# Performance work log

Hardware: AMD Instinct MI355X
Metric: run time of the kernel (lower is better)

The kernel has to match this reference:

```python
import jax, jax.numpy as jnp
import numpy as np

B, S, D = 8, 2048, 512

def setup_inputs() -> dict:
    key = jax.random.key(0)
    ks = jax.random.split(key, 4)
    scale = 1.0 / np.sqrt(D)
    x = jax.random.normal(ks[0], (B, S, D), dtype=jnp.float32)
    Wq = jax.random.normal(ks[1], (D, D), dtype=jnp.float32) * scale
    Wk = jax.random.normal(ks[2], (D, D), dtype=jnp.float32) * scale
    Wv = jax.random.normal(ks[3], (D, D), dtype=jnp.float32) * scale
    bq = jnp.zeros((D,), jnp.float32)
    bk = jnp.zeros((D,), jnp.float32)
    bv = jnp.zeros((D,), jnp.float32)
    return {"x": x, "Wq": Wq, "bq": bq, "Wk": Wk, "bk": bk, "Wv": Wv, "bv": bv}

def reference(x, Wq, bq, Wk, bk, Wv, bv):
    # Q, K, V projections: [B,S,D]
    Q = jnp.einsum('bsd,de->bse', x, Wq) + bq
    K = jnp.einsum('bsd,de->bse', x, Wk) + bk
    V = jnp.einsum('bsd,de->bse', x, Wv) + bv
    scale = jnp.sqrt(jnp.asarray(Q.shape[-1], Q.dtype))
    scores = jnp.einsum('bqd,bkd->bqk', Q, K) / scale  # [B,S,S]
    attn = jax.nn.softmax(scores, axis=-1)
    context = jnp.einsum('bqk,bkd->bqd', attn, V)  # [B,S,D]
    return context
```

## Files before the change

### kernel.cpp

```cpp
#include <hip/hip_runtime.h>
#include <hip/hip_bf16.h>

#define B_ 8
#define S_ 2048
#define D_ 512

typedef __attribute__((ext_vector_type(8))) short short8;
typedef __attribute__((ext_vector_type(4))) float f32x4;

static __device__ __forceinline__ unsigned short f2bf(float f) {
    union { float f; unsigned u; } v; v.f = f;
    unsigned r = v.u + 0x7FFFu + ((v.u >> 16) & 1u);
    return (unsigned short)(r >> 16);
}

static __device__ __forceinline__ float fexp2(float x) {
    float r; asm("v_exp_f32 %0, %1" : "=v"(r) : "v"(x)); return r;
}

static __device__ __forceinline__ void gl_lds16(const void* g, void* l) {
    __builtin_amdgcn_global_load_lds(
        (const __attribute__((address_space(1))) unsigned int*)g,
        (__attribute__((address_space(3))) unsigned int*)l, 16, 0, 0);
}

__global__ void k_prep(const float* __restrict__ x,
                       const float* __restrict__ Wq, const float* __restrict__ Wk,
                       const float* __restrict__ Wv,
                       unsigned short* __restrict__ xb, unsigned short* __restrict__ Wt,
                       float* __restrict__ l) {
    int bid = blockIdx.x;
    if (bid < 4096) {
        int i = bid * 256 + threadIdx.x;
        const float4* p = (const float4*)x + (size_t)i * 2;
        float4 a = p[0], b = p[1];
        union { unsigned short u[8]; uint4 v; } o;
        o.u[0] = f2bf(a.x); o.u[1] = f2bf(a.y); o.u[2] = f2bf(a.z); o.u[3] = f2bf(a.w);
        o.u[4] = f2bf(b.x); o.u[5] = f2bf(b.y); o.u[6] = f2bf(b.z); o.u[7] = f2bf(b.w);
        ((uint4*)xb)[i] = o.v;
    } else if (bid < 7168) {
        int idx = (bid - 4096) * 256 + threadIdx.x;
        int z = idx >> 18;
        int r = idx & 262143;
        int e = r >> 9, d = r & 511;
        const float* W = (z == 0) ? Wq : ((z == 1) ? Wk : Wv);
        Wt[idx] = f2bf(W[d * 512 + e]);
    } else {
        l[(bid - 7168) * 256 + threadIdx.x] = 0.f;
    }
}

__global__ __launch_bounds__(256, 4) void k_qkv(
    const unsigned short* __restrict__ xb, const unsigned short* __restrict__ Wt,
    const float* __restrict__ biasq, const float* __restrict__ biask,
    const float* __restrict__ biasv,
    unsigned short* __restrict__ Qb, unsigned short* __restrict__ Kb,
    unsigned short* __restrict__ Vs) {
  __shared__ __align__(16) unsigned char smA[16384];
  __shared__ __align__(16) unsigned char smB[16384];
  const int z = blockIdx.z;
  const unsigned short* W = Wt + (size_t)z * (D_ * D_);
  const int lane = threadIdx.x & 63, wid = threadIdx.x >> 6;
  const int c = lane & 15, g = lane >> 4;
  const int wr = wid >> 1, wc = wid & 1;
  const int m_blk = blockIdx.x * 128;
  const int n_blk = blockIdx.y * 128;

  const int src_sw = ((lane & 7) * 16) ^ (((lane >> 3) & 7) << 4);
  const unsigned char* ga = (const unsigned char*)xb
      + (size_t)(m_blk + wid * 32 + (lane >> 3)) * 1024;
  const unsigned char* gb = (const unsigned char*)W
      + (size_t)(n_blk + wid * 32 + (lane >> 3)) * 1024;
  unsigned char* la = smA + wid * 4096;
  unsigned char* lb = smB + wid * 4096;

  f32x4 acc[4][4];
#pragma unroll
  for (int mi = 0; mi < 4; ++mi)
#pragma unroll
    for (int ni = 0; ni < 4; ++ni) acc[mi][ni] = (f32x4){0.f, 0.f, 0.f, 0.f};

  for (int step = 0; step < 8; ++step) {
    __syncthreads();
#pragma unroll
    for (int i = 0; i < 4; ++i) {
      gl_lds16(ga + (size_t)i * 8192 + step * 128 + src_sw, la + i * 1024);
      gl_lds16(gb + (size_t)i * 8192 + step * 128 + src_sw, lb + i * 1024);
    }
    __syncthreads();
#pragma unroll
    for (int kc = 0; kc < 2; ++kc) {
      const int ro = (kc * 64 + g * 16) ^ ((c & 7) << 4);
      short8 af[4], bf[4];
#pragma unroll
      for (int mi = 0; mi < 4; ++mi)
        af[mi] = *(const short8*)(smA + (wr * 64 + mi * 16 + c) * 128 + ro);
#pragma unroll
      for (int ni = 0; ni < 4; ++ni)
        bf[ni] = *(const short8*)(smB + (wc * 64 + ni * 16 + c) * 128 + ro);
#pragma unroll
      for (int mi = 0; mi < 4; ++mi)
#pragma unroll
        for (int ni = 0; ni < 4; ++ni)
          acc[mi][ni] = __builtin_amdgcn_mfma_f32_16x16x32_bf16(af[mi], bf[ni], acc[mi][ni], 0, 0, 0);
    }
  }

  const int m0 = m_blk + wr * 64;
  const int n0 = n_blk + wc * 64;
  if (z < 2) {
    const float* bias = (z == 0) ? biasq : biask;
    unsigned short* outp = (z == 0) ? Qb : Kb;
    const float scl = (z == 0) ? 0.0637587238f : 1.0f;
#pragma unroll
    for (int ni = 0; ni < 4; ++ni) {
      int cc = n0 + ni * 16 + c;
      float bb = bias[cc];
#pragma unroll
      for (int mi = 0; mi < 4; ++mi)
#pragma unroll
        for (int r = 0; r < 4; ++r) {
          int row = m0 + mi * 16 + g * 4 + r;
          outp[(size_t)row * D_ + cc] = f2bf((acc[mi][ni][r] + bb) * scl);
        }
    }
  } else {
#pragma unroll
    for (int ni = 0; ni < 4; ++ni) {
      int e = n0 + ni * 16 + c;
      float bb = biasv[e];
#pragma unroll
      for (int mi = 0; mi < 4; ++mi) {
        int row = m0 + mi * 16 + g * 4;
        int bi = row >> 11, sl = row & 2047;
        int t = sl >> 5, kvin = sl & 31;
        union { unsigned short u[4]; uint2 v; } pk;
#pragma unroll
        for (int r = 0; r < 4; ++r) pk.u[r] = f2bf(acc[mi][ni][r] + bb);
        *(uint2*)(Vs + ((((size_t)bi * 64 + t) * 512) + e) * 32 + kvin) = pk.v;
      }
    }
  }
}

__global__ __launch_bounds__(256, 4) void k_pa(
    const unsigned short* __restrict__ Qb, const unsigned short* __restrict__ Kb,
    unsigned short* __restrict__ P, float* __restrict__ l,
    int b_base, int bc) {
  __shared__ __align__(16) unsigned char smA[16384];
  __shared__ __align__(16) unsigned char smB[16384];
  const int lane = threadIdx.x & 63, wid = threadIdx.x >> 6;
  const int c = lane & 15, g = lane >> 4;
  const int wr = wid >> 1, wc = wid & 1;
  const int bloc = blockIdx.x % bc;
  const int tile = blockIdx.x / bc;
  const int b = b_base + bloc;
  const int m_blk = (tile & 15) * 128;
  const int n_blk = (tile >> 4) * 128;
  unsigned short* Pb = P + (size_t)bloc * S_ * S_;

  const int src_sw = ((lane & 7) * 16) ^ (((lane >> 3) & 7) << 4);
  const unsigned char* ga = (const unsigned char*)(Kb + (size_t)b * S_ * D_)
      + (size_t)(m_blk + wid * 32 + (lane >> 3)) * 1024;
  const unsigned char* gb = (const unsigned char*)(Qb + (size_t)b * S_ * D_)
      + (size_t)(n_blk + wid * 32 + (lane >> 3)) * 1024;
  unsigned char* la = smA + wid * 4096;
  unsigned char* lb = smB + wid * 4096;

  f32x4 acc[4][4];
#pragma unroll
  for (int mi = 0; mi < 4; ++mi)
#pragma unroll
    for (int ni = 0; ni < 4; ++ni) acc[mi][ni] = (f32x4){0.f, 0.f, 0.f, 0.f};

  for (int step = 0; step < 8; ++step) {
    __syncthreads();
#pragma unroll
    for (int i = 0; i < 4; ++i) {
      gl_lds16(ga + (size_t)i * 8192 + step * 128 + src_sw, la + i * 1024);
      gl_lds16(gb + (size_t)i * 8192 + step * 128 + src_sw, lb + i * 1024);
    }
    __syncthreads();
#pragma unroll
    for (int kc = 0; kc < 2; ++kc) {
      const int ro = (kc * 64 + g * 16) ^ ((c & 7) << 4);
      short8 af[4], bf[4];
#pragma unroll
      for (int mi = 0; mi < 4; ++mi)
        af[mi] = *(const short8*)(smA + (wr * 64 + mi * 16 + c) * 128 + ro);
#pragma unroll
      for (int ni = 0; ni < 4; ++ni)
        bf[ni] = *(const short8*)(smB + (wc * 64 + ni * 16 + c) * 128 + ro);
#pragma unroll
      for (int mi = 0; mi < 4; ++mi)
#pragma unroll
        for (int ni = 0; ni < 4; ++ni)
          acc[mi][ni] = __builtin_amdgcn_mfma_f32_16x16x32_bf16(af[mi], bf[ni], acc[mi][ni], 0, 0, 0);
    }
  }

  const float SH = 11.5415603f;
  float psum[4] = {0.f, 0.f, 0.f, 0.f};
  __syncthreads();
#pragma unroll
  for (int ni = 0; ni < 4; ++ni) {
    const int q_loc = wc * 64 + ni * 16 + c;
#pragma unroll
    for (int mi = 0; mi < 4; ++mi) {
      float p0 = fexp2(acc[mi][ni][0] - SH);
      float p1 = fexp2(acc[mi][ni][1] - SH);
      float p2 = fexp2(acc[mi][ni][2] - SH);
      float p3 = fexp2(acc[mi][ni][3] - SH);
      psum[ni] += (p0 + p1) + (p2 + p3);
      unsigned w0, w1;
      asm("v_cvt_pk_bf16_f32 %0, %1, %2" : "=v"(w0) : "v"(p0), "v"(p1));
      asm("v_cvt_pk_bf16_f32 %0, %1, %2" : "=v"(w1) : "v"(p2), "v"(p3));
      const int kv2 = (wr * 64 + mi * 16 + g * 4) * 2;
      *(uint2*)(smA + q_loc * 256 + (kv2 ^ ((q_loc & 15) << 4))) = (uint2){w0, w1};
    }
  }
#pragma unroll
  for (int ni = 0; ni < 4; ++ni) {
    float v = psum[ni];
    v += __shfl_xor(v, 16);
    v += __shfl_xor(v, 32);
    if (g == 0)
      atomicAdd(l + b * S_ + n_blk + wc * 64 + ni * 16 + c, v);
  }
  __syncthreads();
#pragma unroll
  for (int i = 0; i < 8; ++i) {
    const int q_loc = wid * 32 + i * 4 + (lane >> 4);
    const int kvb = (lane & 15) * 16;
    uint4 v = *(const uint4*)(smA + q_loc * 256 + (kvb ^ ((q_loc & 15) << 4)));
    *(uint4*)((unsigned char*)Pb + (size_t)(n_blk + q_loc) * 4096 + m_blk * 2 + kvb) = v;
  }
}

__global__ __launch_bounds__(512, 1) void k_pb(
    const unsigned short* __restrict__ P, const unsigned short* __restrict__ Vs,
    const float* __restrict__ l, float* __restrict__ out,
    int b_base, int bc) {
  __shared__ __align__(16) unsigned char sm[147456];
  const int lane = threadIdx.x & 63, wid = threadIdx.x >> 6;
  const int c = lane & 15, g = lane >> 4;
  const int wm = wid >> 2, wn = wid & 3;
  const int bloc = blockIdx.x % bc;
  const int tile = blockIdx.x / bc;
  const int b = b_base + bloc;
  const int m_blk = (tile & 1) * 256;
  const int n_blk = (tile >> 1) * 128;
  const unsigned char* Pb = (const unsigned char*)(P + (size_t)bloc * S_ * S_);
  const unsigned char* Vsb = (const unsigned char*)(Vs + (size_t)b * 64 * 512 * 32);

  const int src_sw = ((lane & 7) * 16) ^ (((lane >> 3) & 7) << 4);
  const unsigned char* gA0 = Vsb + (size_t)(src_sw >> 6) * 32768
      + (size_t)(m_blk + (lane >> 3)) * 64 + (src_sw & 63);
  const unsigned char* gB0 = Pb + (size_t)(n_blk + (lane >> 3)) * 4096 + src_sw;

#define STG_A(h_, t_, bp_)                                                   \
  {                                                                          \
    _Pragma("unroll")                                                        \
    for (int i = 0; i < 2; ++i) {                                            \
      int rl = wid * 16 + i * 8;                                             \
      int pbv = (rl & 63) + ((rl & 64) << 1) + (h_) * 64;                    \
      gl_lds16(gA0 + (size_t)(t_) * 65536 + (size_t)pbv * 64,                \
               sm + (bp_) * 49152 + pbv * 128);                              \
    }                                                                        \
  }
#define STG_B(h_, t_, bp_)                                                   \
  {                                                                          \
    int rl = wid * 8;                                                        \
    int pbv = (rl & 8) + (h_) * 16 + ((rl >> 4) << 5);                       \
    gl_lds16(gB0 + (size_t)pbv * 4096 + (t_) * 128,                          \
             sm + (bp_) * 49152 + 32768 + pbv * 128);                        \
  }

  f32x4 acc[8][2];
#pragma unroll
  for (int a = 0; a < 8; ++a)
#pragma unroll
    for (int ni = 0; ni < 2; ++ni) acc[a][ni] = (f32x4){0.f, 0.f, 0.f, 0.f};

  STG_A(0, 0, 0); STG_B(0, 0, 0); STG_A(1, 0, 0); STG_B(1, 0, 0);
  STG_A(0, 1, 1); STG_B(0, 1, 1); STG_A(1, 1, 1); STG_B(1, 1, 1);

  for (int t = 0; t < 32; ++t) {
    const int cb = t % 3;
    const int nb = (t + 2) % 3;
    if (t < 31) asm volatile("s_waitcnt vmcnt(6)" ::: "memory");
    else        asm volatile("s_waitcnt vmcnt(0)" ::: "memory");
    __builtin_amdgcn_s_barrier();
    const unsigned char* Ab = sm + cb * 49152;
    const unsigned char* Bb = Ab + 32768;
    short8 bfr[2][2];
#pragma unroll
    for (int ni = 0; ni < 2; ++ni) {
      int row = wn * 32 + ni * 16 + c;
#pragma unroll
      for (int kc = 0; kc < 2; ++kc)
        bfr[ni][kc] = *(const short8*)(Bb + row * 128 + ((kc * 64 + g * 16) ^ ((c & 7) << 4)));
    }
    {
      short8 af[4][2];
#pragma unroll
      for (int mi = 0; mi < 4; ++mi) {
        int row = wm * 128 + mi * 16 + c;
#pragma unroll
        for (int kc = 0; kc < 2; ++kc)
          af[mi][kc] = *(const short8*)(Ab + row * 128 + ((kc * 64 + g * 16) ^ ((c & 7) << 4)));
      }
      if (t < 30) { STG_A(0, t + 2, nb); STG_B(0, t + 2, nb); }
      __builtin_amdgcn_s_setprio(1);
#pragma unroll
      for (int kc = 0; kc < 2; ++kc)
#pragma unroll
        for (int mi = 0; mi < 4; ++mi)
#pragma unroll
          for (int ni = 0; ni < 2; ++ni)
            acc[mi][ni] = __builtin_amdgcn_mfma_f32_16x16x32_bf16(af[mi][kc], bfr[ni][kc], acc[mi][ni], 0, 0, 0);
      __builtin_amdgcn_s_setprio(0);
    }
    {
      short8 af[4][2];
#pragma unroll
      for (int mi = 0; mi < 4; ++mi) {
        int row = wm * 128 + 64 + mi * 16 + c;
#pragma unroll
        for (int kc = 0; kc < 2; ++kc)
          af[mi][kc] = *(const short8*)(Ab + row * 128 + ((kc * 64 + g * 16) ^ ((c & 7) << 4)));
      }
      if (t < 30) { STG_A(1, t + 2, nb); STG_B(1, t + 2, nb); }
      __builtin_amdgcn_s_setprio(1);
#pragma unroll
      for (int kc = 0; kc < 2; ++kc)
#pragma unroll
        for (int mi = 0; mi < 4; ++mi)
#pragma unroll
          for (int ni = 0; ni < 2; ++ni)
            acc[4 + mi][ni] = __builtin_amdgcn_mfma_f32_16x16x32_bf16(af[mi][kc], bfr[ni][kc], acc[4 + mi][ni], 0, 0, 0);
      __builtin_amdgcn_s_setprio(0);
    }
  }
#undef STG_A
#undef STG_B

  float* ob = out + (size_t)b * S_ * D_;
#pragma unroll
  for (int ni = 0; ni < 2; ++ni) {
    const int q = n_blk + wn * 32 + ni * 16 + c;
    const float inv = 1.f / l[b * S_ + q];
#pragma unroll
    for (int a = 0; a < 8; ++a) {
      const int d0 = m_blk + wm * 128 + (a >> 2) * 64 + (a & 3) * 16 + g * 4;
      float4 v;
      v.x = acc[a][ni][0] * inv; v.y = acc[a][ni][1] * inv;
      v.z = acc[a][ni][2] * inv; v.w = acc[a][ni][3] * inv;
      *(float4*)(ob + (size_t)q * D_ + d0) = v;
    }
  }
}

extern "C" void kernel_launch(void* const* d_in, const int* in_sizes, int n_in,
                              void* d_out, int out_size, void* d_ws, size_t ws_size,
                              hipStream_t stream) {
  const float* x  = (const float*)d_in[0];
  const float* Wq = (const float*)d_in[1];
  const float* bq = (const float*)d_in[2];
  const float* Wk = (const float*)d_in[3];
  const float* bk = (const float*)d_in[4];
  const float* Wv = (const float*)d_in[5];
  const float* bv = (const float*)d_in[6];
  float* out = (float*)d_out;

  unsigned short* xb = (unsigned short*)d_ws;
  unsigned short* Wt = xb + (size_t)16384 * 512;
  unsigned short* Qb = Wt + (size_t)3 * 512 * 512;
  unsigned short* Kb = Qb + (size_t)16384 * 512;
  unsigned short* Vs = Kb + (size_t)16384 * 512;
  float* l = (float*)(Vs + (size_t)8 * 64 * 512 * 32);
  unsigned short* Pfull = (unsigned short*)(l + 8 * 2048);
  const size_t full_need =
      (size_t)((unsigned char*)(Pfull + (size_t)8 * 2048 * 2048) - (unsigned char*)d_ws);

  k_prep<<<dim3(7232), dim3(256), 0, stream>>>(x, Wq, Wk, Wv, xb, Wt, l);
  k_qkv<<<dim3(128, 4, 3), dim3(256), 0, stream>>>(xb, Wt, bq, bk, bv, Qb, Kb, Vs);

  if (ws_size >= full_need) {
    k_pa<<<dim3(2048), dim3(256), 0, stream>>>(Qb, Kb, Pfull, l, 0, 8);
    k_pb<<<dim3(256),  dim3(512), 0, stream>>>(Pfull, Vs, l, out, 0, 8);
  } else {
    unsigned short* P2 = xb;
    for (int g2 = 0; g2 < 4; ++g2) {
      k_pa<<<dim3(512), dim3(256), 0, stream>>>(Qb, Kb, P2, l, g2 * 2, 2);
      k_pb<<<dim3(64), dim3(512), 0, stream>>>(P2, Vs, l, out, g2 * 2, 2);
    }
  }
}
```

Baseline: 119.5 us.

## Restructure score kernel to 256x128 tiles with triple-buffered async LDS pipeline

The QK^T/exp kernel moves from 128x128 tiles on 256-thread blocks with two barriers per K-step to 256x128 tiles on 512-thread blocks. K and Q chunks are loaded into a three-stage LDS ring with global-to-LDS copies issued two steps ahead, and partial vmcnt waits keep loads in flight. It also raises MFMA priority around the math bursts. The goal is to hide global load latency and improve reuse per block, at the cost of one block per CU with about 144KB of LDS and lower occupancy.

```diff
diff --git a/kernel.cpp b/kernel.cpp
--- a/kernel.cpp
+++ b/kernel.cpp
@@ -143,96 +143,146 @@
   }
 }
 
-__global__ __launch_bounds__(256, 4) void k_pa(
+__global__ __launch_bounds__(512, 1) void k_pa(
     const unsigned short* __restrict__ Qb, const unsigned short* __restrict__ Kb,
     unsigned short* __restrict__ P, float* __restrict__ l,
     int b_base, int bc) {
-  __shared__ __align__(16) unsigned char smA[16384];
-  __shared__ __align__(16) unsigned char smB[16384];
+  __shared__ __align__(16) unsigned char sm[147456];
   const int lane = threadIdx.x & 63, wid = threadIdx.x >> 6;
   const int c = lane & 15, g = lane >> 4;
-  const int wr = wid >> 1, wc = wid & 1;
+  const int wm = wid >> 2, wn = wid & 3;
   const int bloc = blockIdx.x % bc;
   const int tile = blockIdx.x / bc;
   const int b = b_base + bloc;
-  const int m_blk = (tile & 15) * 128;
-  const int n_blk = (tile >> 4) * 128;
+  const int m_blk = (tile & 7) * 256;
+  const int n_blk = (tile >> 3) * 128;
   unsigned short* Pb = P + (size_t)bloc * S_ * S_;
 
   const int src_sw = ((lane & 7) * 16) ^ (((lane >> 3) & 7) << 4);
-  const unsigned char* ga = (const unsigned char*)(Kb + (size_t)b * S_ * D_)
-      + (size_t)(m_blk + wid * 32 + (lane >> 3)) * 1024;
-  const unsigned char* gb = (const unsigned char*)(Qb + (size_t)b * S_ * D_)
-      + (size_t)(n_blk + wid * 32 + (lane >> 3)) * 1024;
-  unsigned char* la = smA + wid * 4096;
-  unsigned char* lb = smB + wid * 4096;
-
-  f32x4 acc[4][4];
-#pragma unroll
-  for (int mi = 0; mi < 4; ++mi)
-#pragma unroll
-    for (int ni = 0; ni < 4; ++ni) acc[mi][ni] = (f32x4){0.f, 0.f, 0.f, 0.f};
-
-  for (int step = 0; step < 8; ++step) {
-    __syncthreads();
-#pragma unroll
-    for (int i = 0; i < 4; ++i) {
-      gl_lds16(ga + (size_t)i * 8192 + step * 128 + src_sw, la + i * 1024);
-      gl_lds16(gb + (size_t)i * 8192 + step * 128 + src_sw, lb + i * 1024);
-    }
-    __syncthreads();
-#pragma unroll
-    for (int kc = 0; kc < 2; ++kc) {
-      const int ro = (kc * 64 + g * 16) ^ ((c & 7) << 4);
-      short8 af[4], bf[4];
-#pragma unroll
-      for (int mi = 0; mi < 4; ++mi)
-        af[mi] = *(const short8*)(smA + (wr * 64 + mi * 16 + c) * 128 + ro);
-#pragma unroll
-      for (int ni = 0; ni < 4; ++ni)
-        bf[ni] = *(const short8*)(smB + (wc * 64 + ni * 16 + c) * 128 + ro);
-#pragma unroll
-      for (int mi = 0; mi < 4; ++mi)
-#pragma unroll
-        for (int ni = 0; ni < 4; ++ni)
-          acc[mi][ni] = __builtin_amdgcn_mfma_f32_16x16x32_bf16(af[mi], bf[ni], acc[mi][ni], 0, 0, 0);
-    }
-  }
-
+  const unsigned char* gA0 = (const unsigned char*)(Kb + (size_t)b * S_ * D_)
+      + (size_t)(m_blk + (lane >> 3)) * 1024 + src_sw;
+  const unsigned char* gB0 = (const unsigned char*)(Qb + (size_t)b * S_ * D_)
+      + (size_t)(n_blk + (lane >> 3)) * 1024 + src_sw;
+
+#define STG_A(h_, t_, bp_)                                                   \
+  {                                                                          \
+    _Pragma("unroll")                                                        \
+    for (int i = 0; i < 2; ++i) {                                            \
+      int r0 = (h_) * 128 + wid * 16 + i * 8;                                \
+      gl_lds16(gA0 + (size_t)r0 * 1024 + (t_) * 128,                         \
+               sm + (bp_) * 49152 + r0 * 128);                               \
+    }                                                                        \
+  }
+#define STG_B(h_, t_, bp_)                                                   \
+  {                                                                          \
+    int r0 = (h_) * 64 + wid * 8;                                            \
+    gl_lds16(gB0 + (size_t)r0 * 1024 + (t_) * 128,                           \
+             sm + (bp_) * 49152 + 32768 + r0 * 128);                         \
+  }
+
+  f32x4 acc[8][2];
+#pragma unroll
+  for (int a = 0; a < 8; ++a)
+#pragma unroll
+    for (int ni = 0; ni < 2; ++ni) acc[a][ni] = (f32x4){0.f, 0.f, 0.f, 0.f};
+
+  STG_A(0, 0, 0); STG_B(0, 0, 0); STG_A(1, 0, 0); STG_B(1, 0, 0);
+  STG_A(0, 1, 1); STG_B(0, 1, 1); STG_A(1, 1, 1); STG_B(1, 1, 1);
+
+  for (int t = 0; t < 8; ++t) {
+    const int cb = t % 3;
+    const int nb = (t + 2) % 3;
+    if (t < 7) asm volatile("s_waitcnt vmcnt(6)" ::: "memory");
+    else       asm volatile("s_waitcnt vmcnt(0)" ::: "memory");
+    __builtin_amdgcn_s_barrier();
+    const unsigned char* Ab = sm + cb * 49152;
+    const unsigned char* Bb = Ab + 32768;
+    short8 bfr[2][2];
+#pragma unroll
+    for (int ni = 0; ni < 2; ++ni) {
+      int row = wn * 32 + ni * 16 + c;
+#pragma unroll
+      for (int kc = 0; kc < 2; ++kc)
+        bfr[ni][kc] = *(const short8*)(Bb + row * 128 + ((kc * 64 + g * 16) ^ ((c & 7) << 4)));
+    }
+    {
+      short8 af[4][2];
+#pragma unroll
+      for (int mi = 0; mi < 4; ++mi) {
+        int row = wm * 128 + mi * 16 + c;
+#pragma unroll
+        for (int kc = 0; kc < 2; ++kc)
+          af[mi][kc] = *(const short8*)(Ab + row * 128 + ((kc * 64 + g * 16) ^ ((c & 7) << 4)));
+      }
+      if (t < 6) { STG_A(0, t + 2, nb); STG_B(0, t + 2, nb); }
+      __builtin_amdgcn_s_setprio(1);
+#pragma unroll
+      for (int kc = 0; kc < 2; ++kc)
+#pragma unroll
+        for (int mi = 0; mi < 4; ++mi)
+#pragma unroll
+          for (int ni = 0; ni < 2; ++ni)
+            acc[mi][ni] = __builtin_amdgcn_mfma_f32_16x16x32_bf16(af[mi][kc], bfr[ni][kc], acc[mi][ni], 0, 0, 0);
+      __builtin_amdgcn_s_setprio(0);
+    }
+    {
+      short8 af[4][2];
+#pragma unroll
+      for (int mi = 0; mi < 4; ++mi) {
+        int row = wm * 128 + 64 + mi * 16 + c;
+#pragma unroll
+        for (int kc = 0; kc < 2; ++kc)
+          af[mi][kc] = *(const short8*)(Ab + row * 128 + ((kc * 64 + g * 16) ^ ((c & 7) << 4)));
+      }
+      if (t < 6) { STG_A(1, t + 2, nb); STG_B(1, t + 2, nb); }
+      __builtin_amdgcn_s_setprio(1);
+#pragma unroll
+      for (int kc = 0; kc < 2; ++kc)
+#pragma unroll
+        for (int mi = 0; mi < 4; ++mi)
+#pragma unroll
+          for (int ni = 0; ni < 2; ++ni)
+            acc[4 + mi][ni] = __builtin_amdgcn_mfma_f32_16x16x32_bf16(af[mi][kc], bfr[ni][kc], acc[4 + mi][ni], 0, 0, 0);
+      __builtin_amdgcn_s_setprio(0);
+    }
+  }
+#undef STG_A
+#undef STG_B
+
+  __syncthreads();
   const float SH = 11.5415603f;
-  float psum[4] = {0.f, 0.f, 0.f, 0.f};
-  __syncthreads();
-#pragma unroll
-  for (int ni = 0; ni < 4; ++ni) {
-    const int q_loc = wc * 64 + ni * 16 + c;
-#pragma unroll
-    for (int mi = 0; mi < 4; ++mi) {
-      float p0 = fexp2(acc[mi][ni][0] - SH);
-      float p1 = fexp2(acc[mi][ni][1] - SH);
-      float p2 = fexp2(acc[mi][ni][2] - SH);
-      float p3 = fexp2(acc[mi][ni][3] - SH);
+  float psum[2] = {0.f, 0.f};
+#pragma unroll
+  for (int ni = 0; ni < 2; ++ni) {
+    const int q_loc = wn * 32 + ni * 16 + c;
+#pragma unroll
+    for (int a = 0; a < 8; ++a) {
+      float p0 = fexp2(acc[a][ni][0] - SH);
+      float p1 = fexp2(acc[a][ni][1] - SH);
+      float p2 = fexp2(acc[a][ni][2] - SH);
+      float p3 = fexp2(acc[a][ni][3] - SH);
       psum[ni] += (p0 + p1) + (p2 + p3);
       unsigned w0, w1;
       asm("v_cvt_pk_bf16_f32 %0, %1, %2" : "=v"(w0) : "v"(p0), "v"(p1));
       asm("v_cvt_pk_bf16_f32 %0, %1, %2" : "=v"(w1) : "v"(p2), "v"(p3));
-      const int kv2 = (wr * 64 + mi * 16 + g * 4) * 2;
-      *(uint2*)(smA + q_loc * 256 + (kv2 ^ ((q_loc & 15) << 4))) = (uint2){w0, w1};
-    }
-  }
-#pragma unroll
-  for (int ni = 0; ni < 4; ++ni) {
+      const int kv2 = wm * 256 + (a >> 2) * 128 + (a & 3) * 32 + g * 8;
+      *(uint2*)(sm + q_loc * 512 + (kv2 ^ ((q_loc & 15) << 4))) = (uint2){w0, w1};
+    }
+  }
+#pragma unroll
+  for (int ni = 0; ni < 2; ++ni) {
     float v = psum[ni];
     v += __shfl_xor(v, 16);
     v += __shfl_xor(v, 32);
     if (g == 0)
-      atomicAdd(l + b * S_ + n_blk + wc * 64 + ni * 16 + c, v);
+      atomicAdd(l + b * S_ + n_blk + wn * 32 + ni * 16 + c, v);
   }
   __syncthreads();
 #pragma unroll
   for (int i = 0; i < 8; ++i) {
-    const int q_loc = wid * 32 + i * 4 + (lane >> 4);
-    const int kvb = (lane & 15) * 16;
-    uint4 v = *(const uint4*)(smA + q_loc * 256 + (kvb ^ ((q_loc & 15) << 4)));
+    const int q_loc = wid * 16 + i * 2 + (lane >> 5);
+    const int kvb = (lane & 31) * 16;
+    uint4 v = *(const uint4*)(sm + q_loc * 512 + (kvb ^ ((q_loc & 15) << 4)));
     *(uint4*)((unsigned char*)Pb + (size_t)(n_blk + q_loc) * 4096 + m_blk * 2 + kvb) = v;
   }
 }
@@ -387,12 +437,12 @@
   k_qkv<<<dim3(128, 4, 3), dim3(256), 0, stream>>>(xb, Wt, bq, bk, bv, Qb, Kb, Vs);
 
   if (ws_size >= full_need) {
-    k_pa<<<dim3(2048), dim3(256), 0, stream>>>(Qb, Kb, Pfull, l, 0, 8);
+    k_pa<<<dim3(1024), dim3(512), 0, stream>>>(Qb, Kb, Pfull, l, 0, 8);
     k_pb<<<dim3(256),  dim3(512), 0, stream>>>(Pfull, Vs, l, out, 0, 8);
   } else {
     unsigned short* P2 = xb;
     for (int g2 = 0; g2 < 4; ++g2) {
-      k_pa<<<dim3(512), dim3(256), 0, stream>>>(Qb, Kb, P2, l, g2 * 2, 2);
+      k_pa<<<dim3(256), dim3(512), 0, stream>>>(Qb, Kb, P2, l, g2 * 2, 2);
       k_pb<<<dim3(64), dim3(512), 0, stream>>>(P2, Vs, l, out, g2 * 2, 2);
     }
   }
```

After: 123.4 us. 1.03x slower.
